# Performance work log

Hardware: AMD Instinct MI355X
Metric: run time of the kernel (lower is better)

## Reference

```python
import jax, jax.numpy as jnp
import numpy as np

B = 1048576
VEC_SZ = 4
LUT_BITS = 8
K = 2 ** LUT_BITS  # 256 codewords


def setup_inputs() -> dict:
    key = jax.random.key(0)
    kx, kt = jax.random.split(key)
    X = jax.random.normal(kx, (B, VEC_SZ), dtype=jnp.float32)
    tlut = jax.random.normal(kt, (K, VEC_SZ), dtype=jnp.float32)  # codebook [K, vec_sz]
    return {"X": X, "tlut": tlut}


def reference(X, tlut):
    # torch.cdist(X, tlut) -> argmin is equivalent to argmin of squared distances:
    x_sq = jnp.sum(X * X, axis=-1, keepdims=True)            # [B, 1]
    c_sq = jnp.sum(tlut * tlut, axis=-1)                     # [K]
    cross = jnp.einsum('bd,kd->bk', X, tlut)                 # [B, K]
    dist2 = x_sq - 2.0 * cross + c_sq                        # [B, K]
    state = jnp.argmin(dist2, axis=-1).astype(jnp.int32)     # [B]
    hatX = jnp.take(tlut, state, axis=0)                     # gather reconstruction [B, vec_sz]
    return hatX, state
```

## Files before the change

### kernel.cpp

```cpp
#include <hip/hip_runtime.h>

#define K_CW 256
#define PPT 4
#define NQ 4
#define KQ (K_CW / NQ)

struct P8 { float4 a; float4 b; };

__global__ void vq_pack_kernel(const float* __restrict__ tlut, float* __restrict__ pk) {
    int k = threadIdx.x;
    float c0 = tlut[k * 4 + 0];
    float c1 = tlut[k * 4 + 1];
    float c2 = tlut[k * 4 + 2];
    float c3 = tlut[k * 4 + 3];
    float s = __fadd_rn(__fadd_rn(__fadd_rn(__fmul_rn(c0, c0), __fmul_rn(c1, c1)),
                                  __fmul_rn(c2, c2)),
                        __fmul_rn(c3, c3));
    pk[k * 8 + 0] = c0; pk[k * 8 + 1] = c1; pk[k * 8 + 2] = c2; pk[k * 8 + 3] = c3;
    pk[k * 8 + 4] = s;  pk[k * 8 + 5] = 0.f; pk[k * 8 + 6] = 0.f; pk[k * 8 + 7] = 0.f;
}

__global__ __launch_bounds__(1024, 8) void vq_argmin_kernel(
    const float* __restrict__ X,
    const float* __restrict__ tlut,
    const float* __restrict__ pk,
    float* __restrict__ outX,
    float* __restrict__ outS,
    int B) {
    __shared__ float4 sd[3 * 256];
    __shared__ int4   si[3 * 256];

    const int t = threadIdx.x;
    const int tt = t & 255;
    const int q = t >> 8;
    const int kbase = __builtin_amdgcn_readfirstlane(q << 6);

    const int g = blockIdx.x * 256 + tt;
    const int stride = B / PPT;

    const float4* __restrict__ X4 = reinterpret_cast<const float4*>(X);
    const float4* __restrict__ T4 = reinterpret_cast<const float4*>(tlut);
    const P8* __restrict__ PK = reinterpret_cast<const P8*>(pk);

    float x0[PPT], x1[PPT], x2[PPT], x3[PPT], xsq[PPT], bestd[PPT];
    int besti[PPT];

    #pragma unroll
    for (int i = 0; i < PPT; ++i) {
        const float4 xv = X4[g + i * stride];
        x0[i] = xv.x; x1[i] = xv.y; x2[i] = xv.z; x3[i] = xv.w;
        xsq[i] = __fadd_rn(__fadd_rn(__fadd_rn(__fmul_rn(xv.x, xv.x), __fmul_rn(xv.y, xv.y)),
                                     __fmul_rn(xv.z, xv.z)),
                           __fmul_rn(xv.w, xv.w));
        bestd[i] = __builtin_inff();
        besti[i] = kbase;
    }

    #pragma unroll 16
    for (int kk = 0; kk < KQ; ++kk) {
        const int k = kbase + kk;
        const P8 e = PK[k];
        const float4 c = e.a;
        const float cs = e.b.x;
        #pragma unroll
        for (int i = 0; i < PPT; ++i) {
            float cross = __fmul_rn(x0[i], c.x);
            cross = __fmaf_rn(x1[i], c.y, cross);
            cross = __fmaf_rn(x2[i], c.z, cross);
            cross = __fmaf_rn(x3[i], c.w, cross);
            float t2 = __fmaf_rn(-2.0f, cross, xsq[i]);
            float d = __fadd_rn(t2, cs);
            besti[i] = (d < bestd[i]) ? k : besti[i];
            bestd[i] = fminf(d, bestd[i]);
        }
    }

    if (q > 0) {
        sd[(q - 1) * 256 + tt] = make_float4(bestd[0], bestd[1], bestd[2], bestd[3]);
        si[(q - 1) * 256 + tt] = make_int4(besti[0], besti[1], besti[2], besti[3]);
    }
    __syncthreads();
    if (q == 0) {
        #pragma unroll
        for (int j = 0; j < 3; ++j) {
            const float4 od = sd[j * 256 + tt];
            const int4   oi = si[j * 256 + tt];
            if (od.x < bestd[0]) { bestd[0] = od.x; besti[0] = oi.x; }
            if (od.y < bestd[1]) { bestd[1] = od.y; besti[1] = oi.y; }
            if (od.z < bestd[2]) { bestd[2] = od.z; besti[2] = oi.z; }
            if (od.w < bestd[3]) { bestd[3] = od.w; besti[3] = oi.w; }
        }
        #pragma unroll
        for (int i = 0; i < PPT; ++i) {
            const int p = g + i * stride;
            reinterpret_cast<float4*>(outX)[p] = T4[besti[i]];
            outS[p] = (float)besti[i];
        }
    }
}

extern "C" void kernel_launch(void* const* d_in, const int* in_sizes, int n_in,
                              void* d_out, int out_size, void* d_ws, size_t ws_size,
                              hipStream_t stream) {
    const float* X    = (const float*)d_in[0];
    const float* tlut = (const float*)d_in[1];
    const int B = in_sizes[0] / 4;

    float* outX = (float*)d_out;
    float* outS = outX + (size_t)B * 4;

    float* pk = (float*)d_ws;

    vq_pack_kernel<<<1, 256, 0, stream>>>(tlut, pk);

    const int groups = B / PPT;
    const int grid = groups / 256;
    vq_argmin_kernel<<<grid, 1024, 0, stream>>>(X, tlut, pk, outX, outS, B);
}
```

Baseline: 116.6 us.

## Drop split-K shared-memory reduction; each thread scans all codewords with prefetch

Replaces the 4-way split of the codebook across thread quarters, and the LDS reduction with its barrier, by having each thread scan all 256 codewords for 2 points instead of 4. Codebook entries are double-buffered in registers, so the next group of 4 entries is loaded while the current group is computed. Blocks shrink to 256 threads and the grid doubles. This removes the shared memory traffic and __syncthreads, but each thread now runs a 256-step serial loop and reuses each loaded codeword across fewer points.

Measured after the change: 127.2 us. 1.09x slower.

```diff
diff --git a/kernel.cpp b/kernel.cpp
--- a/kernel.cpp
+++ b/kernel.cpp
@@ -1,9 +1,7 @@
 #include <hip/hip_runtime.h>
 
 #define K_CW 256
-#define PPT 4
-#define NQ 4
-#define KQ (K_CW / NQ)
+#define PPT 2
 
 struct P8 { float4 a; float4 b; };
 
@@ -20,22 +18,31 @@
     pk[k * 8 + 4] = s;  pk[k * 8 + 5] = 0.f; pk[k * 8 + 6] = 0.f; pk[k * 8 + 7] = 0.f;
 }
 
-__global__ __launch_bounds__(1024, 8) void vq_argmin_kernel(
+#define VQ_STEP(E, KIDX)                                                     \
+    do {                                                                     \
+        const float4 c_ = (E).a;                                             \
+        const float cs_ = (E).b.x;                                           \
+        _Pragma("unroll")                                                    \
+        for (int i_ = 0; i_ < PPT; ++i_) {                                   \
+            float cr_ = __fmul_rn(x0[i_], c_.x);                             \
+            cr_ = __fmaf_rn(x1[i_], c_.y, cr_);                              \
+            cr_ = __fmaf_rn(x2[i_], c_.z, cr_);                              \
+            cr_ = __fmaf_rn(x3[i_], c_.w, cr_);                              \
+            float t2_ = __fmaf_rn(-2.0f, cr_, xsq[i_]);                      \
+            float d_ = __fadd_rn(t2_, cs_);                                  \
+            besti[i_] = (d_ < bestd[i_]) ? (KIDX) : besti[i_];               \
+            bestd[i_] = fminf(d_, bestd[i_]);                                \
+        }                                                                    \
+    } while (0)
+
+__global__ __launch_bounds__(256, 8) void vq_argmin_kernel(
     const float* __restrict__ X,
     const float* __restrict__ tlut,
     const float* __restrict__ pk,
     float* __restrict__ outX,
     float* __restrict__ outS,
     int B) {
-    __shared__ float4 sd[3 * 256];
-    __shared__ int4   si[3 * 256];
-
-    const int t = threadIdx.x;
-    const int tt = t & 255;
-    const int q = t >> 8;
-    const int kbase = __builtin_amdgcn_readfirstlane(q << 6);
-
-    const int g = blockIdx.x * 256 + tt;
+    const int g = blockIdx.x * 256 + threadIdx.x;
     const int stride = B / PPT;
 
     const float4* __restrict__ X4 = reinterpret_cast<const float4*>(X);
@@ -53,49 +60,30 @@
                                      __fmul_rn(xv.z, xv.z)),
                            __fmul_rn(xv.w, xv.w));
         bestd[i] = __builtin_inff();
-        besti[i] = kbase;
+        besti[i] = 0;
     }
 
-    #pragma unroll 16
-    for (int kk = 0; kk < KQ; ++kk) {
-        const int k = kbase + kk;
-        const P8 e = PK[k];
-        const float4 c = e.a;
-        const float cs = e.b.x;
+    P8 b0[4], b1[4];
+    #pragma unroll
+    for (int j = 0; j < 4; ++j) b0[j] = PK[j];
+
+    #pragma unroll 2
+    for (int kk = 0; kk < K_CW; kk += 8) {
         #pragma unroll
-        for (int i = 0; i < PPT; ++i) {
-            float cross = __fmul_rn(x0[i], c.x);
-            cross = __fmaf_rn(x1[i], c.y, cross);
-            cross = __fmaf_rn(x2[i], c.z, cross);
-            cross = __fmaf_rn(x3[i], c.w, cross);
-            float t2 = __fmaf_rn(-2.0f, cross, xsq[i]);
-            float d = __fadd_rn(t2, cs);
-            besti[i] = (d < bestd[i]) ? k : besti[i];
-            bestd[i] = fminf(d, bestd[i]);
-        }
+        for (int j = 0; j < 4; ++j) b1[j] = PK[kk + 4 + j];
+        #pragma unroll
+        for (int j = 0; j < 4; ++j) VQ_STEP(b0[j], kk + j);
+        #pragma unroll
+        for (int j = 0; j < 4; ++j) b0[j] = PK[(kk + 8 + j) & (K_CW - 1)];
+        #pragma unroll
+        for (int j = 0; j < 4; ++j) VQ_STEP(b1[j], kk + 4 + j);
     }
 
-    if (q > 0) {
-        sd[(q - 1) * 256 + tt] = make_float4(bestd[0], bestd[1], bestd[2], bestd[3]);
-        si[(q - 1) * 256 + tt] = make_int4(besti[0], besti[1], besti[2], besti[3]);
-    }
-    __syncthreads();
-    if (q == 0) {
-        #pragma unroll
-        for (int j = 0; j < 3; ++j) {
-            const float4 od = sd[j * 256 + tt];
-            const int4   oi = si[j * 256 + tt];
-            if (od.x < bestd[0]) { bestd[0] = od.x; besti[0] = oi.x; }
-            if (od.y < bestd[1]) { bestd[1] = od.y; besti[1] = oi.y; }
-            if (od.z < bestd[2]) { bestd[2] = od.z; besti[2] = oi.z; }
-            if (od.w < bestd[3]) { bestd[3] = od.w; besti[3] = oi.w; }
-        }
-        #pragma unroll
-        for (int i = 0; i < PPT; ++i) {
-            const int p = g + i * stride;
-            reinterpret_cast<float4*>(outX)[p] = T4[besti[i]];
-            outS[p] = (float)besti[i];
-        }
+    #pragma unroll
+    for (int i = 0; i < PPT; ++i) {
+        const int p = g + i * stride;
+        reinterpret_cast<float4*>(outX)[p] = T4[besti[i]];
+        outS[p] = (float)besti[i];
     }
 }
 
@@ -115,5 +103,5 @@
 
     const int groups = B / PPT;
     const int grid = groups / 256;
-    vq_argmin_kernel<<<grid, 1024, 0, stream>>>(X, tlut, pk, outX, outS, B);
+    vq_argmin_kernel<<<grid, 256, 0, stream>>>(X, tlut, pk, outX, outS, B);
 }
```

## Stage codebook in LDS per block and drop split-K reduction and pack kernel

Applied to the files above, without the earlier changes.

Each 256-thread block loads the codebook into shared memory and computes codeword norms in place, removing the separate pack kernel launch. Each thread now scans all 256 codewords for two points instead of splitting the codebook across four wave groups, eliminating the shared-memory cross-group argmin reduction and its barrier. The reconstruction gather reads from LDS instead of global memory. In exchange, every block redoes codebook staging, and inner-loop codeword reads become LDS broadcasts rather than uniform global/scalar loads.

New measurement: 119.5 us. +2.5%, slower.

```diff
diff --git a/kernel.cpp b/kernel.cpp
--- a/kernel.cpp
+++ b/kernel.cpp
@@ -1,46 +1,33 @@
 #include <hip/hip_runtime.h>
 
 #define K_CW 256
-#define PPT 4
-#define NQ 4
-#define KQ (K_CW / NQ)
+#define PPT 2
 
-struct P8 { float4 a; float4 b; };
-
-__global__ void vq_pack_kernel(const float* __restrict__ tlut, float* __restrict__ pk) {
-    int k = threadIdx.x;
-    float c0 = tlut[k * 4 + 0];
-    float c1 = tlut[k * 4 + 1];
-    float c2 = tlut[k * 4 + 2];
-    float c3 = tlut[k * 4 + 3];
-    float s = __fadd_rn(__fadd_rn(__fadd_rn(__fmul_rn(c0, c0), __fmul_rn(c1, c1)),
-                                  __fmul_rn(c2, c2)),
-                        __fmul_rn(c3, c3));
-    pk[k * 8 + 0] = c0; pk[k * 8 + 1] = c1; pk[k * 8 + 2] = c2; pk[k * 8 + 3] = c3;
-    pk[k * 8 + 4] = s;  pk[k * 8 + 5] = 0.f; pk[k * 8 + 6] = 0.f; pk[k * 8 + 7] = 0.f;
-}
-
-__global__ __launch_bounds__(1024, 8) void vq_argmin_kernel(
+__global__ __launch_bounds__(256, 8) void vq_argmin_kernel(
     const float* __restrict__ X,
     const float* __restrict__ tlut,
-    const float* __restrict__ pk,
     float* __restrict__ outX,
     float* __restrict__ outS,
     int B) {
-    __shared__ float4 sd[3 * 256];
-    __shared__ int4   si[3 * 256];
+    __shared__ float4 sc[K_CW];
+    __shared__ float  ss[K_CW];
 
     const int t = threadIdx.x;
-    const int tt = t & 255;
-    const int q = t >> 8;
-    const int kbase = __builtin_amdgcn_readfirstlane(q << 6);
 
-    const int g = blockIdx.x * 256 + tt;
+    {
+        const float4 cv = reinterpret_cast<const float4*>(tlut)[t];
+        const float s = __fadd_rn(__fadd_rn(__fadd_rn(__fmul_rn(cv.x, cv.x),
+                                                      __fmul_rn(cv.y, cv.y)),
+                                            __fmul_rn(cv.z, cv.z)),
+                                  __fmul_rn(cv.w, cv.w));
+        sc[t] = cv;
+        ss[t] = s;
+    }
+
+    const int g = blockIdx.x * 256 + t;
     const int stride = B / PPT;
 
     const float4* __restrict__ X4 = reinterpret_cast<const float4*>(X);
-    const float4* __restrict__ T4 = reinterpret_cast<const float4*>(tlut);
-    const P8* __restrict__ PK = reinterpret_cast<const P8*>(pk);
 
     float x0[PPT], x1[PPT], x2[PPT], x3[PPT], xsq[PPT], bestd[PPT];
     int besti[PPT];
@@ -53,15 +40,15 @@
                                      __fmul_rn(xv.z, xv.z)),
                            __fmul_rn(xv.w, xv.w));
         bestd[i] = __builtin_inff();
-        besti[i] = kbase;
+        besti[i] = 0;
     }
 
-    #pragma unroll 16
-    for (int kk = 0; kk < KQ; ++kk) {
-        const int k = kbase + kk;
-        const P8 e = PK[k];
-        const float4 c = e.a;
-        const float cs = e.b.x;
+    __syncthreads();
+
+    #pragma unroll 8
+    for (int k = 0; k < K_CW; ++k) {
+        const float4 c = sc[k];
+        const float cs = ss[k];
         #pragma unroll
         for (int i = 0; i < PPT; ++i) {
             float cross = __fmul_rn(x0[i], c.x);
@@ -75,27 +62,11 @@
         }
     }
 
-    if (q > 0) {
-        sd[(q - 1) * 256 + tt] = make_float4(bestd[0], bestd[1], bestd[2], bestd[3]);
-        si[(q - 1) * 256 + tt] = make_int4(besti[0], besti[1], besti[2], besti[3]);
-    }
-    __syncthreads();
-    if (q == 0) {
-        #pragma unroll
-        for (int j = 0; j < 3; ++j) {
-            const float4 od = sd[j * 256 + tt];
-            const int4   oi = si[j * 256 + tt];
-            if (od.x < bestd[0]) { bestd[0] = od.x; besti[0] = oi.x; }
-            if (od.y < bestd[1]) { bestd[1] = od.y; besti[1] = oi.y; }
-            if (od.z < bestd[2]) { bestd[2] = od.z; besti[2] = oi.z; }
-            if (od.w < bestd[3]) { bestd[3] = od.w; besti[3] = oi.w; }
-        }
-        #pragma unroll
-        for (int i = 0; i < PPT; ++i) {
-            const int p = g + i * stride;
-            reinterpret_cast<float4*>(outX)[p] = T4[besti[i]];
-            outS[p] = (float)besti[i];
-        }
+    #pragma unroll
+    for (int i = 0; i < PPT; ++i) {
+        const int p = g + i * stride;
+        reinterpret_cast<float4*>(outX)[p] = sc[besti[i]];
+        outS[p] = (float)besti[i];
     }
 }
 
@@ -109,11 +80,7 @@
     float* outX = (float*)d_out;
     float* outS = outX + (size_t)B * 4;
 
-    float* pk = (float*)d_ws;
-
-    vq_pack_kernel<<<1, 256, 0, stream>>>(tlut, pk);
-
     const int groups = B / PPT;
     const int grid = groups / 256;
-    vq_argmin_kernel<<<grid, 1024, 0, stream>>>(X, tlut, pk, outX, outS, B);
+    vq_argmin_kernel<<<grid, 256, 0, stream>>>(X, tlut, outX, outS, B);
 }
```

## Scan full codebook per thread instead of splitting across four thread groups

Applied to the files above, without the earlier changes.

Each thread now evaluates all 256 codewords for its four points, replacing the four-way codeword split across 1024-thread blocks. This removes the shared-memory partial-result exchange, the block barrier and the idle three quarters of threads during output writes. In exchange there are four times fewer threads, so fewer waves are resident to hide latency and the per-thread serial loop is four times longer.

Measured after the change: 128.9 us. 1.11x slower.

```diff
diff --git a/kernel.cpp b/kernel.cpp
--- a/kernel.cpp
+++ b/kernel.cpp
@@ -2,8 +2,6 @@
 
 #define K_CW 256
 #define PPT 4
-#define NQ 4
-#define KQ (K_CW / NQ)
 
 struct P8 { float4 a; float4 b; };
 
@@ -20,22 +18,14 @@
     pk[k * 8 + 4] = s;  pk[k * 8 + 5] = 0.f; pk[k * 8 + 6] = 0.f; pk[k * 8 + 7] = 0.f;
 }
 
-__global__ __launch_bounds__(1024, 8) void vq_argmin_kernel(
+__global__ __launch_bounds__(256, 4) void vq_argmin_kernel(
     const float* __restrict__ X,
     const float* __restrict__ tlut,
     const float* __restrict__ pk,
     float* __restrict__ outX,
     float* __restrict__ outS,
     int B) {
-    __shared__ float4 sd[3 * 256];
-    __shared__ int4   si[3 * 256];
-
-    const int t = threadIdx.x;
-    const int tt = t & 255;
-    const int q = t >> 8;
-    const int kbase = __builtin_amdgcn_readfirstlane(q << 6);
-
-    const int g = blockIdx.x * 256 + tt;
+    const int g = blockIdx.x * 256 + threadIdx.x;
     const int stride = B / PPT;
 
     const float4* __restrict__ X4 = reinterpret_cast<const float4*>(X);
@@ -53,12 +43,11 @@
                                      __fmul_rn(xv.z, xv.z)),
                            __fmul_rn(xv.w, xv.w));
         bestd[i] = __builtin_inff();
-        besti[i] = kbase;
+        besti[i] = 0;
     }
 
     #pragma unroll 16
-    for (int kk = 0; kk < KQ; ++kk) {
-        const int k = kbase + kk;
+    for (int k = 0; k < K_CW; ++k) {
         const P8 e = PK[k];
         const float4 c = e.a;
         const float cs = e.b.x;
@@ -75,27 +64,11 @@
         }
     }
 
-    if (q > 0) {
-        sd[(q - 1) * 256 + tt] = make_float4(bestd[0], bestd[1], bestd[2], bestd[3]);
-        si[(q - 1) * 256 + tt] = make_int4(besti[0], besti[1], besti[2], besti[3]);
-    }
-    __syncthreads();
-    if (q == 0) {
-        #pragma unroll
-        for (int j = 0; j < 3; ++j) {
-            const float4 od = sd[j * 256 + tt];
-            const int4   oi = si[j * 256 + tt];
-            if (od.x < bestd[0]) { bestd[0] = od.x; besti[0] = oi.x; }
-            if (od.y < bestd[1]) { bestd[1] = od.y; besti[1] = oi.y; }
-            if (od.z < bestd[2]) { bestd[2] = od.z; besti[2] = oi.z; }
-            if (od.w < bestd[3]) { bestd[3] = od.w; besti[3] = oi.w; }
-        }
-        #pragma unroll
-        for (int i = 0; i < PPT; ++i) {
-            const int p = g + i * stride;
-            reinterpret_cast<float4*>(outX)[p] = T4[besti[i]];
-            outS[p] = (float)besti[i];
-        }
+    #pragma unroll
+    for (int i = 0; i < PPT; ++i) {
+        const int p = g + i * stride;
+        reinterpret_cast<float4*>(outX)[p] = T4[besti[i]];
+        outS[p] = (float)besti[i];
     }
 }
 
@@ -115,5 +88,5 @@
 
     const int groups = B / PPT;
     const int grid = groups / 256;
-    vq_argmin_kernel<<<grid, 1024, 0, stream>>>(X, tlut, pk, outX, outS, B);
+    vq_argmin_kernel<<<grid, 256, 0, stream>>>(X, tlut, pk, outX, outS, B);
 }
```
